# Performance work log

Measured on AMD Instinct MI355X. Metric: run time of the kernel, lower is better.

## Reference

```python
import jax, jax.numpy as jnp
import numpy as np

B, N, K = 8, 4096, 20          # clouds, points per cloud, knn neighbors
IN_C, OUT_C = 3, 64            # xyz coords -> feature channels


def setup_inputs() -> dict:
    key = jax.random.key(0)
    k1, k2 = jax.random.split(key, 2)
    x = jax.random.normal(k1, (B * N, IN_C), dtype=jnp.float32)
    batch = (jnp.arange(B * N, dtype=jnp.int32) // N)  # [0..0,1..1,...] equal-size clouds
    # EdgeConv MLP: Linear(2*in_channels -> out_channels) + ReLU
    W = jax.random.normal(k2, (2 * IN_C, OUT_C), dtype=jnp.float32) / jnp.sqrt(jnp.float32(2 * IN_C))
    b = jnp.zeros((OUT_C,), dtype=jnp.float32)
    return {"x": x, "batch": batch, "W": W, "b": b}


def _knn_idx(xr):
    # xr: [B, N, C] -> neighbor indices [B, N, K] (self excluded, like knn_graph loop=False)
    sq = jnp.sum(xr * xr, axis=-1)                                  # [B, N]
    d = sq[:, :, None] + sq[:, None, :] - 2.0 * jnp.einsum("bnd,bmd->bnm", xr, xr)  # [B,N,N]
    ar = jnp.arange(N)
    d = d.at[:, ar, ar].set(jnp.inf)                                 # exclude self-loops
    _, idx = jax.lax.top_k(-d, K)                                    # k smallest distances
    return idx


def reference(x, batch, W, b):
    # batch encodes B equal-size clouds of N points each (constant structure)
    xr = x.reshape(B, N, IN_C)
    idx = _knn_idx(xr)                                               # [B, N, K]
    x_j = jax.vmap(lambda pts, i: pts[i])(xr, idx)                   # gather neighbors [B,N,K,C]
    x_i = xr[:, :, None, :]                                          # center points   [B,N,1,C]
    msg = jnp.concatenate([jnp.broadcast_to(x_i, x_j.shape), x_j - x_i], axis=-1)  # [B,N,K,2C]
    h = jax.nn.relu(jnp.einsum("bnkc,co->bnko", msg, W) + b)         # EdgeConv MLP
    out = jnp.max(h, axis=2)                                         # max aggregation over K
    return out.reshape(B * N, OUT_C)
```

## Files before the change

### kernel.cpp

```cpp
#include <hip/hip_runtime.h>
#include <math.h>

#define NN    4096
#define KK    20
#define QQ    4
#define WAVES 4
#define BLK   (WAVES*64)
#define PPB   (WAVES*QQ)
#define PIT   16
#define CAP   56
#define BPB   (NN/PPB)
#define BB    8

typedef float f32x4 __attribute__((ext_vector_type(4)));
typedef float f32x2 __attribute__((ext_vector_type(2)));

__device__ __forceinline__ unsigned fkey(float f) {
  unsigned u = __float_as_uint(f);
  return u ^ ((unsigned)((int)u >> 31) | 0x80000000u);
}
__device__ __forceinline__ float fkey_inv(unsigned k) {
  unsigned u = (k & 0x80000000u) ? (k ^ 0x80000000u) : ~k;
  return __uint_as_float(u);
}

__global__ void prep_kernel(const float* __restrict__ x,
                            float4* __restrict__ ws4,
                            f32x4* __restrict__ wspk) {
  const int p = blockIdx.x * 256 + threadIdx.x;
  const float* s = x + (size_t)p * 6;
  const float x0 = s[0], y0 = s[1], z0 = s[2];
  const float x1 = s[3], y1 = s[4], z1 = s[5];
  const float w0 = fmaf(z0, z0, fmaf(y0, y0, x0 * x0));
  const float w1 = fmaf(z1, z1, fmaf(y1, y1, x1 * x1));
  ws4[2 * p]     = make_float4(x0, y0, z0, w0);
  ws4[2 * p + 1] = make_float4(x1, y1, z1, w1);
  wspk[2 * p]     = (f32x4){x0, x1, y0, y1};
  wspk[2 * p + 1] = (f32x4){z0, z1, w0, w1};
}

template<bool WS>
__global__ __launch_bounds__(BLK, 8)
void edgeconv_kernel(const float* __restrict__ x,
                     const float4* __restrict__ ws4,
                     const f32x4* __restrict__ wspk,
                     const float* __restrict__ W,
                     const float* __restrict__ bias,
                     float* __restrict__ out) {
  __shared__ float2 cand[PPB][CAP + 1];
  __shared__ int    jkeep[PPB][21];
  __shared__ int    pc[PPB];
  __shared__ int    pk[PPB];

  const int tid  = threadIdx.x;
  const int lane = tid & 63;
  const int w    = tid >> 6;
  const int bb   = blockIdx.x / BPB;
  const int blk  = blockIdx.x % BPB;
  const int base = bb * NN;
  const int g0   = w * QQ;
  const int myp0 = blk * PPB + g0;

  f32x2 nxp[QQ], nyp[QQ], nzp[QQ];
  #pragma unroll
  for (int q = 0; q < QQ; ++q) {
    const float* p = x + (size_t)(base + myp0 + q) * 3;
    const float a = -2.f * p[0], b = -2.f * p[1], c = -2.f * p[2];
    nxp[q] = (f32x2){a, a}; nyp[q] = (f32x2){b, b}; nzp[q] = (f32x2){c, c};
  }

  if (tid < PPB) { pc[tid] = 0; pk[tid] = 0; }
  __syncthreads();

  auto ldpair = [&](int pr, f32x4& A, f32x4& Bv) {
    if constexpr (WS) {
      A  = wspk[base + (pr << 1)];
      Bv = wspk[base + (pr << 1) + 1];
    } else {
      const float* s = x + ((size_t)base + ((size_t)pr << 1)) * 3;
      const float x0 = s[0], y0 = s[1], z0 = s[2];
      const float x1 = s[3], y1 = s[4], z1 = s[5];
      A  = (f32x4){x0, x1, y0, y1};
      Bv = (f32x4){z0, z1, fmaf(z0, z0, fmaf(y0, y0, x0 * x0)),
                           fmaf(z1, z1, fmaf(y1, y1, x1 * x1))};
    }
  };
  auto ldp = [&](int j) -> float4 {
    if constexpr (WS) {
      return ws4[base + j];
    } else {
      const float* p = x + (size_t)(base + j) * 3;
      const float a = p[0], b = p[1], c = p[2];
      return make_float4(a, b, c, fmaf(c, c, fmaf(b, b, a * a)));
    }
  };
  auto pdist = [&](int q, const f32x4& A, const f32x4& Bv) -> f32x2 {
    return __builtin_elementwise_fma(nxp[q], A.xy,
            __builtin_elementwise_fma(nyp[q], A.zw,
             __builtin_elementwise_fma(nzp[q], Bv.xy, Bv.zw)));
  };

  float m[QQ];
  #pragma unroll
  for (int q = 0; q < QQ; ++q) m[q] = INFINITY;
  #pragma unroll 1
  for (int i = 0; i < PIT; ++i) {
    f32x4 A0, B0, A1, B1;
    ldpair((2 * i + 0) * 64 + lane, A0, B0);
    ldpair((2 * i + 1) * 64 + lane, A1, B1);
    #pragma unroll
    for (int q = 0; q < QQ; ++q) {
      const f32x2 dA = pdist(q, A0, B0);
      const f32x2 dB = pdist(q, A1, B1);
      m[q] = fminf(fminf(m[q], fminf(dA.x, dA.y)), fminf(dB.x, dB.y));
    }
  }

  float tau[QQ];
  #pragma unroll
  for (int q = 0; q < QQ; ++q) {
    const unsigned key = fkey(m[q]);
    unsigned lo = 0u, hi = 0xFFFFFFFFu;
    for (int b = 0; b < 32; ++b) {
      const unsigned mid = lo + ((hi - lo) >> 1);
      const unsigned long long bal = __ballot(key <= mid);
      if (__popcll(bal) > KK) hi = mid; else lo = mid + 1;
    }
    tau[q] = fkey_inv(lo);
  }

  #pragma unroll 1
  for (int i = 0; i < PIT; ++i) {
    const int pr0 = (2 * i + 0) * 64 + lane;
    const int pr1 = (2 * i + 1) * 64 + lane;
    f32x4 A0, B0, A1, B1;
    ldpair(pr0, A0, B0);
    ldpair(pr1, A1, B1);
    #pragma unroll
    for (int q = 0; q < QQ; ++q) {
      const f32x2 dA = pdist(q, A0, B0);
      const f32x2 dB = pdist(q, A1, B1);
      if (fminf(dA.x, dA.y) <= tau[q]) {
        if (dA.x <= tau[q]) { const int wp = atomicAdd(&pc[g0 + q], 1);
          if (wp < CAP) cand[g0 + q][wp] = make_float2(dA.x, __int_as_float(2 * pr0)); }
        if (dA.y <= tau[q]) { const int wp = atomicAdd(&pc[g0 + q], 1);
          if (wp < CAP) cand[g0 + q][wp] = make_float2(dA.y, __int_as_float(2 * pr0 + 1)); }
      }
      if (fminf(dB.x, dB.y) <= tau[q]) {
        if (dB.x <= tau[q]) { const int wp = atomicAdd(&pc[g0 + q], 1);
          if (wp < CAP) cand[g0 + q][wp] = make_float2(dB.x, __int_as_float(2 * pr1)); }
        if (dB.y <= tau[q]) { const int wp = atomicAdd(&pc[g0 + q], 1);
          if (wp < CAP) cand[g0 + q][wp] = make_float2(dB.y, __int_as_float(2 * pr1 + 1)); }
      }
    }
  }
  __syncthreads();

  {
    const int g   = tid >> 4;
    const int k0  = tid & 15;
    const int myp = blk * PPB + g;
    const int n0  = pc[g];
    const int n   = n0 < CAP ? n0 : CAP;
    for (int k = k0; k < n; k += 16) {
      const float2 ck = cand[g][k];
      const float dk = ck.x; const int jk = __float_as_int(ck.y);
      int rank = 0;
      for (int k2 = 0; k2 < n; ++k2) {
        const float2 c2 = cand[g][k2];
        rank += (c2.x < dk || (c2.x == dk && __float_as_int(c2.y) < jk)) ? 1 : 0;
      }
      if (jk != myp && rank <= KK) jkeep[g][atomicAdd(&pk[g], 1)] = jk;
    }
  }
  __syncthreads();

  const float w3 = W[3*64+lane], w4 = W[4*64+lane], w5 = W[5*64+lane];
  const float c0 = W[0*64+lane] - w3;
  const float c1 = W[1*64+lane] - w4;
  const float c2 = W[2*64+lane] - w5;
  const float bo = bias[lane];

  for (int pi = 0; pi < QQ; ++pi) {
    const int p   = g0 + pi;
    const int pid = blk * PPB + p;
    const float4 xi = ldp(pid);
    const float ci = fmaf(xi.x, c0, fmaf(xi.y, c1, fmaf(xi.z, c2, bo)));
    float hmax = -INFINITY;
    #pragma unroll 5
    for (int k = 0; k < KK; ++k) {
      const int j = __builtin_amdgcn_readfirstlane(jkeep[p][k]);
      const float4 xp = ldp(j);
      hmax = fmaxf(hmax, fmaf(xp.x, w3, fmaf(xp.y, w4, fmaf(xp.z, w5, ci))));
    }
    out[(size_t)(base + pid) * 64 + lane] = fmaxf(hmax, 0.0f);
  }
}

extern "C" void kernel_launch(void* const* d_in, const int* in_sizes, int n_in,
                              void* d_out, int out_size, void* d_ws, size_t ws_size,
                              hipStream_t stream) {
  const float* x  = (const float*)d_in[0];
  const float* W  = (const float*)d_in[2];
  const float* b  = (const float*)d_in[3];
  float* out = (float*)d_out;

  const size_t aosz = (size_t)BB * NN * sizeof(float4);
  const size_t need = 2 * aosz;
  dim3 grid(BB * BPB);
  dim3 block(BLK);
  if (ws_size >= need) {
    float4* ws4 = (float4*)d_ws;
    f32x4* wspk = (f32x4*)((char*)d_ws + aosz);
    hipLaunchKernelGGL(prep_kernel, dim3(BB * NN / 2 / 256), dim3(256), 0, stream,
                       x, ws4, wspk);
    hipLaunchKernelGGL((edgeconv_kernel<true>), grid, block, 0, stream,
                       x, ws4, wspk, W, b, out);
  } else {
    hipLaunchKernelGGL((edgeconv_kernel<false>), grid, block, 0, stream,
                       x, (const float4*)nullptr, (const f32x4*)nullptr, W, b, out);
  }
}
```

Before: 76.66 us.

## Stage whole cloud into LDS, double block size, compact candidate keys

Each block now copies its cloud's packed point pairs (64 KB) into shared memory once and runs both distance passes out of LDS instead of global/L2. The block grows to 8 waves (32 query points) so that staging cost is spread over more queries, and launch bounds drop to 4 blocks per SM. Candidates are stored as a sortable uint key plus a 16-bit index, so ranking becomes a single 64-bit compare, and CAP is reduced to 48. The risks are lower occupancy from the large LDS footprint and more candidate overflow with the smaller CAP.

```diff
diff --git a/kernel.cpp b/kernel.cpp
--- a/kernel.cpp
+++ b/kernel.cpp
@@ -4,11 +4,12 @@
 #define NN    4096
 #define KK    20
 #define QQ    4
-#define WAVES 4
+#define WAVES 8
 #define BLK   (WAVES*64)
 #define PPB   (WAVES*QQ)
+#define NPAIR (NN/2)
 #define PIT   16
-#define CAP   56
+#define CAP   48
 #define BPB   (NN/PPB)
 #define BB    8
 
@@ -26,7 +27,8 @@
 
 __global__ void prep_kernel(const float* __restrict__ x,
                             float4* __restrict__ ws4,
-                            f32x4* __restrict__ wspk) {
+                            f32x4* __restrict__ wsA,
+                            f32x4* __restrict__ wsB) {
   const int p = blockIdx.x * 256 + threadIdx.x;
   const float* s = x + (size_t)p * 6;
   const float x0 = s[0], y0 = s[1], z0 = s[2];
@@ -35,28 +37,32 @@
   const float w1 = fmaf(z1, z1, fmaf(y1, y1, x1 * x1));
   ws4[2 * p]     = make_float4(x0, y0, z0, w0);
   ws4[2 * p + 1] = make_float4(x1, y1, z1, w1);
-  wspk[2 * p]     = (f32x4){x0, x1, y0, y1};
-  wspk[2 * p + 1] = (f32x4){z0, z1, w0, w1};
+  wsA[p] = (f32x4){x0, x1, y0, y1};
+  wsB[p] = (f32x4){z0, z1, w0, w1};
 }
 
 template<bool WS>
-__global__ __launch_bounds__(BLK, 8)
+__global__ __launch_bounds__(BLK, 4)
 void edgeconv_kernel(const float* __restrict__ x,
                      const float4* __restrict__ ws4,
-                     const f32x4* __restrict__ wspk,
+                     const f32x4* __restrict__ wsA,
+                     const f32x4* __restrict__ wsB,
                      const float* __restrict__ W,
                      const float* __restrict__ bias,
                      float* __restrict__ out) {
-  __shared__ float2 cand[PPB][CAP + 1];
-  __shared__ int    jkeep[PPB][21];
-  __shared__ int    pc[PPB];
-  __shared__ int    pk[PPB];
+  __shared__ f32x4 ldsA[NPAIR];
+  __shared__ f32x4 ldsB[NPAIR];
+  __shared__ unsigned       ckey[PPB][CAP + 1];
+  __shared__ unsigned short cj[PPB][CAP + 2];
+  __shared__ int jkeep[PPB][21];
+  __shared__ int pc[PPB];
+  __shared__ int pk[PPB];
 
   const int tid  = threadIdx.x;
   const int lane = tid & 63;
   const int w    = tid >> 6;
-  const int bb   = blockIdx.x / BPB;
-  const int blk  = blockIdx.x % BPB;
+  const int bb   = blockIdx.x >> 7;
+  const int blk  = blockIdx.x & (BPB - 1);
   const int base = bb * NN;
   const int g0   = w * QQ;
   const int myp0 = blk * PPB + g0;
@@ -69,21 +75,30 @@
     nxp[q] = (f32x2){a, a}; nyp[q] = (f32x2){b, b}; nzp[q] = (f32x2){c, c};
   }
 
+  if constexpr (WS) {
+    #pragma unroll
+    for (int t = tid; t < NPAIR; t += BLK) {
+      ldsA[t] = wsA[bb * NPAIR + t];
+      ldsB[t] = wsB[bb * NPAIR + t];
+    }
+  } else {
+    #pragma unroll
+    for (int t = tid; t < NPAIR; t += BLK) {
+      const float* s = x + ((size_t)base + 2 * (size_t)t) * 3;
+      const float x0 = s[0], y0 = s[1], z0 = s[2];
+      const float x1 = s[3], y1 = s[4], z1 = s[5];
+      ldsA[t] = (f32x4){x0, x1, y0, y1};
+      ldsB[t] = (f32x4){z0, z1, fmaf(z0, z0, fmaf(y0, y0, x0 * x0)),
+                                fmaf(z1, z1, fmaf(y1, y1, x1 * x1))};
+    }
+  }
   if (tid < PPB) { pc[tid] = 0; pk[tid] = 0; }
   __syncthreads();
 
-  auto ldpair = [&](int pr, f32x4& A, f32x4& Bv) {
-    if constexpr (WS) {
-      A  = wspk[base + (pr << 1)];
-      Bv = wspk[base + (pr << 1) + 1];
-    } else {
-      const float* s = x + ((size_t)base + ((size_t)pr << 1)) * 3;
-      const float x0 = s[0], y0 = s[1], z0 = s[2];
-      const float x1 = s[3], y1 = s[4], z1 = s[5];
-      A  = (f32x4){x0, x1, y0, y1};
-      Bv = (f32x4){z0, z1, fmaf(z0, z0, fmaf(y0, y0, x0 * x0)),
-                           fmaf(z1, z1, fmaf(y1, y1, x1 * x1))};
-    }
+  auto pdist = [&](int q, const f32x4& A, const f32x4& Bv) -> f32x2 {
+    return __builtin_elementwise_fma(nxp[q], A.xy,
+            __builtin_elementwise_fma(nyp[q], A.zw,
+             __builtin_elementwise_fma(nzp[q], Bv.xy, Bv.zw)));
   };
   auto ldp = [&](int j) -> float4 {
     if constexpr (WS) {
@@ -94,20 +109,16 @@
       return make_float4(a, b, c, fmaf(c, c, fmaf(b, b, a * a)));
     }
   };
-  auto pdist = [&](int q, const f32x4& A, const f32x4& Bv) -> f32x2 {
-    return __builtin_elementwise_fma(nxp[q], A.xy,
-            __builtin_elementwise_fma(nyp[q], A.zw,
-             __builtin_elementwise_fma(nzp[q], Bv.xy, Bv.zw)));
-  };
 
   float m[QQ];
   #pragma unroll
   for (int q = 0; q < QQ; ++q) m[q] = INFINITY;
   #pragma unroll 1
   for (int i = 0; i < PIT; ++i) {
-    f32x4 A0, B0, A1, B1;
-    ldpair((2 * i + 0) * 64 + lane, A0, B0);
-    ldpair((2 * i + 1) * 64 + lane, A1, B1);
+    const f32x4 A0 = ldsA[(2 * i + 0) * 64 + lane];
+    const f32x4 B0 = ldsB[(2 * i + 0) * 64 + lane];
+    const f32x4 A1 = ldsA[(2 * i + 1) * 64 + lane];
+    const f32x4 B1 = ldsB[(2 * i + 1) * 64 + lane];
     #pragma unroll
     for (int q = 0; q < QQ; ++q) {
       const f32x2 dA = pdist(q, A0, B0);
@@ -133,25 +144,22 @@
   for (int i = 0; i < PIT; ++i) {
     const int pr0 = (2 * i + 0) * 64 + lane;
     const int pr1 = (2 * i + 1) * 64 + lane;
-    f32x4 A0, B0, A1, B1;
-    ldpair(pr0, A0, B0);
-    ldpair(pr1, A1, B1);
+    const f32x4 A0 = ldsA[pr0];
+    const f32x4 B0 = ldsB[pr0];
+    const f32x4 A1 = ldsA[pr1];
+    const f32x4 B1 = ldsB[pr1];
     #pragma unroll
     for (int q = 0; q < QQ; ++q) {
       const f32x2 dA = pdist(q, A0, B0);
       const f32x2 dB = pdist(q, A1, B1);
-      if (fminf(dA.x, dA.y) <= tau[q]) {
-        if (dA.x <= tau[q]) { const int wp = atomicAdd(&pc[g0 + q], 1);
-          if (wp < CAP) cand[g0 + q][wp] = make_float2(dA.x, __int_as_float(2 * pr0)); }
-        if (dA.y <= tau[q]) { const int wp = atomicAdd(&pc[g0 + q], 1);
-          if (wp < CAP) cand[g0 + q][wp] = make_float2(dA.y, __int_as_float(2 * pr0 + 1)); }
-      }
-      if (fminf(dB.x, dB.y) <= tau[q]) {
-        if (dB.x <= tau[q]) { const int wp = atomicAdd(&pc[g0 + q], 1);
-          if (wp < CAP) cand[g0 + q][wp] = make_float2(dB.x, __int_as_float(2 * pr1)); }
-        if (dB.y <= tau[q]) { const int wp = atomicAdd(&pc[g0 + q], 1);
-          if (wp < CAP) cand[g0 + q][wp] = make_float2(dB.y, __int_as_float(2 * pr1 + 1)); }
-      }
+      if (dA.x <= tau[q]) { const int wp = atomicAdd(&pc[g0 + q], 1);
+        if (wp < CAP) { ckey[g0 + q][wp] = fkey(dA.x); cj[g0 + q][wp] = 2 * pr0; } }
+      if (dA.y <= tau[q]) { const int wp = atomicAdd(&pc[g0 + q], 1);
+        if (wp < CAP) { ckey[g0 + q][wp] = fkey(dA.y); cj[g0 + q][wp] = 2 * pr0 + 1; } }
+      if (dB.x <= tau[q]) { const int wp = atomicAdd(&pc[g0 + q], 1);
+        if (wp < CAP) { ckey[g0 + q][wp] = fkey(dB.x); cj[g0 + q][wp] = 2 * pr1; } }
+      if (dB.y <= tau[q]) { const int wp = atomicAdd(&pc[g0 + q], 1);
+        if (wp < CAP) { ckey[g0 + q][wp] = fkey(dB.y); cj[g0 + q][wp] = 2 * pr1 + 1; } }
     }
   }
   __syncthreads();
@@ -163,12 +171,14 @@
     const int n0  = pc[g];
     const int n   = n0 < CAP ? n0 : CAP;
     for (int k = k0; k < n; k += 16) {
-      const float2 ck = cand[g][k];
-      const float dk = ck.x; const int jk = __float_as_int(ck.y);
+      const unsigned long long me =
+          ((unsigned long long)ckey[g][k] << 16) | cj[g][k];
+      const int jk = (int)(me & 0xFFFFu);
       int rank = 0;
       for (int k2 = 0; k2 < n; ++k2) {
-        const float2 c2 = cand[g][k2];
-        rank += (c2.x < dk || (c2.x == dk && __float_as_int(c2.y) < jk)) ? 1 : 0;
+        const unsigned long long o =
+            ((unsigned long long)ckey[g][k2] << 16) | cj[g][k2];
+        rank += (o < me) ? 1 : 0;
       }
       if (jk != myp && rank <= KK) jkeep[g][atomicAdd(&pk[g], 1)] = jk;
     }
@@ -206,18 +216,21 @@
   float* out = (float*)d_out;
 
   const size_t aosz = (size_t)BB * NN * sizeof(float4);
-  const size_t need = 2 * aosz;
+  const size_t prsz = (size_t)BB * NPAIR * sizeof(float4);
+  const size_t need = aosz + 2 * prsz;
   dim3 grid(BB * BPB);
   dim3 block(BLK);
   if (ws_size >= need) {
     float4* ws4 = (float4*)d_ws;
-    f32x4* wspk = (f32x4*)((char*)d_ws + aosz);
+    f32x4* wsA = (f32x4*)((char*)d_ws + aosz);
+    f32x4* wsB = (f32x4*)((char*)d_ws + aosz + prsz);
     hipLaunchKernelGGL(prep_kernel, dim3(BB * NN / 2 / 256), dim3(256), 0, stream,
-                       x, ws4, wspk);
+                       x, ws4, wsA, wsB);
     hipLaunchKernelGGL((edgeconv_kernel<true>), grid, block, 0, stream,
-                       x, ws4, wspk, W, b, out);
+                       x, ws4, wsA, wsB, W, b, out);
   } else {
     hipLaunchKernelGGL((edgeconv_kernel<false>), grid, block, 0, stream,
-                       x, (const float4*)nullptr, (const f32x4*)nullptr, W, b, out);
-  }
-}
+                       x, (const float4*)nullptr, (const f32x4*)nullptr,
+                       (const f32x4*)nullptr, W, b, out);
+  }
+}
```

Result: slower. 90.60 us (+18.2%).

## Double waves per block, interleave clouds across blocks, sync waves per stripe

Applied to the files above, without the earlier changes.

Raises the block to 8 waves (32 queries per block), so each block handles more query points over the same candidate stream. Block-to-cloud mapping is interleaved so neighbouring blocks work on different clouds. The two scan passes are split into four stripes with a block barrier after each, keeping the waves in step so the shared x data stays hot in cache. The threshold bisection exits early once exactly K+1 keys fall under mid and takes the max such key via shuffles. The branch guarding candidate insertion is removed. The trade-off is barrier cost, fewer blocks in the grid, and higher LDS use per block.

```diff
diff --git a/kernel.cpp b/kernel.cpp
--- a/kernel.cpp
+++ b/kernel.cpp
@@ -4,10 +4,12 @@
 #define NN    4096
 #define KK    20
 #define QQ    4
-#define WAVES 4
+#define WAVES 8
 #define BLK   (WAVES*64)
 #define PPB   (WAVES*QQ)
 #define PIT   16
+#define STR   4
+#define SPI   (PIT/STR)
 #define CAP   56
 #define BPB   (NN/PPB)
 #define BB    8
@@ -55,8 +57,8 @@
   const int tid  = threadIdx.x;
   const int lane = tid & 63;
   const int w    = tid >> 6;
-  const int bb   = blockIdx.x / BPB;
-  const int blk  = blockIdx.x % BPB;
+  const int bb   = blockIdx.x % BB;
+  const int blk  = blockIdx.x / BB;
   const int base = bb * NN;
   const int g0   = w * QQ;
   const int myp0 = blk * PPB + g0;
@@ -104,57 +106,71 @@
   #pragma unroll
   for (int q = 0; q < QQ; ++q) m[q] = INFINITY;
   #pragma unroll 1
-  for (int i = 0; i < PIT; ++i) {
-    f32x4 A0, B0, A1, B1;
-    ldpair((2 * i + 0) * 64 + lane, A0, B0);
-    ldpair((2 * i + 1) * 64 + lane, A1, B1);
-    #pragma unroll
-    for (int q = 0; q < QQ; ++q) {
-      const f32x2 dA = pdist(q, A0, B0);
-      const f32x2 dB = pdist(q, A1, B1);
-      m[q] = fminf(fminf(m[q], fminf(dA.x, dA.y)), fminf(dB.x, dB.y));
-    }
+  for (int st = 0; st < STR; ++st) {
+    #pragma unroll 1
+    for (int ii = 0; ii < SPI; ++ii) {
+      const int i = st * SPI + ii;
+      f32x4 A0, B0, A1, B1;
+      ldpair((2 * i + 0) * 64 + lane, A0, B0);
+      ldpair((2 * i + 1) * 64 + lane, A1, B1);
+      #pragma unroll
+      for (int q = 0; q < QQ; ++q) {
+        const f32x2 dA = pdist(q, A0, B0);
+        const f32x2 dB = pdist(q, A1, B1);
+        m[q] = fminf(fminf(m[q], fminf(dA.x, dA.y)), fminf(dB.x, dB.y));
+      }
+    }
+    __syncthreads();
   }
 
   float tau[QQ];
   #pragma unroll
   for (int q = 0; q < QQ; ++q) {
     const unsigned key = fkey(m[q]);
-    unsigned lo = 0u, hi = 0xFFFFFFFFu;
+    unsigned lo = 0u, hi = 0xFFFFFFFFu, res = 0u;
     for (int b = 0; b < 32; ++b) {
       const unsigned mid = lo + ((hi - lo) >> 1);
-      const unsigned long long bal = __ballot(key <= mid);
-      if (__popcll(bal) > KK) hi = mid; else lo = mid + 1;
-    }
-    tau[q] = fkey_inv(lo);
+      const int cnt = __popcll(__ballot(key <= mid));
+      if (cnt == KK + 1) {
+        unsigned t = (key <= mid) ? key : 0u;
+        #pragma unroll
+        for (int s = 32; s; s >>= 1) {
+          const unsigned o = (unsigned)__shfl_xor((int)t, s, 64);
+          t = t > o ? t : o;
+        }
+        res = t; break;
+      }
+      if (cnt > KK) hi = mid; else lo = mid + 1;
+    }
+    tau[q] = fkey_inv(res ? res : lo);
   }
 
   #pragma unroll 1
-  for (int i = 0; i < PIT; ++i) {
-    const int pr0 = (2 * i + 0) * 64 + lane;
-    const int pr1 = (2 * i + 1) * 64 + lane;
-    f32x4 A0, B0, A1, B1;
-    ldpair(pr0, A0, B0);
-    ldpair(pr1, A1, B1);
-    #pragma unroll
-    for (int q = 0; q < QQ; ++q) {
-      const f32x2 dA = pdist(q, A0, B0);
-      const f32x2 dB = pdist(q, A1, B1);
-      if (fminf(dA.x, dA.y) <= tau[q]) {
+  for (int st = 0; st < STR; ++st) {
+    #pragma unroll 1
+    for (int ii = 0; ii < SPI; ++ii) {
+      const int i = st * SPI + ii;
+      const int pr0 = (2 * i + 0) * 64 + lane;
+      const int pr1 = (2 * i + 1) * 64 + lane;
+      f32x4 A0, B0, A1, B1;
+      ldpair(pr0, A0, B0);
+      ldpair(pr1, A1, B1);
+      #pragma unroll
+      for (int q = 0; q < QQ; ++q) {
+        const f32x2 dA = pdist(q, A0, B0);
+        const f32x2 dB = pdist(q, A1, B1);
         if (dA.x <= tau[q]) { const int wp = atomicAdd(&pc[g0 + q], 1);
           if (wp < CAP) cand[g0 + q][wp] = make_float2(dA.x, __int_as_float(2 * pr0)); }
         if (dA.y <= tau[q]) { const int wp = atomicAdd(&pc[g0 + q], 1);
           if (wp < CAP) cand[g0 + q][wp] = make_float2(dA.y, __int_as_float(2 * pr0 + 1)); }
-      }
-      if (fminf(dB.x, dB.y) <= tau[q]) {
         if (dB.x <= tau[q]) { const int wp = atomicAdd(&pc[g0 + q], 1);
           if (wp < CAP) cand[g0 + q][wp] = make_float2(dB.x, __int_as_float(2 * pr1)); }
         if (dB.y <= tau[q]) { const int wp = atomicAdd(&pc[g0 + q], 1);
           if (wp < CAP) cand[g0 + q][wp] = make_float2(dB.y, __int_as_float(2 * pr1 + 1)); }
       }
     }
-  }
-  __syncthreads();
+    __syncthreads();
+  }
 
   {
     const int g   = tid >> 4;
```

Result: slower. 83.82 us (+9.3%).
